# Performance work log

Hardware: AMD Instinct MI355X
Metric: run time of the kernel (lower is better)

Reference implementation:

```python
import jax, jax.numpy as jnp
import numpy as np

HEADS = 4


def setup_inputs() -> dict:
    key = jax.random.key(0)
    kx, kqkv, kbq, ko, kbo = jax.random.split(key, 5)
    B, C, H, W = 4, 256, 64, 64
    x = jax.random.normal(kx, (B, C, H, W), dtype=jnp.float32)
    # torch nn.Linear stores weight as [out_features, in_features]
    w_qkv = jax.random.normal(kqkv, (3 * C, C), dtype=jnp.float32) * (1.0 / np.sqrt(C))
    b_qkv = jax.random.normal(kbq, (3 * C,), dtype=jnp.float32) * 0.02
    w_o = jax.random.normal(ko, (C, C), dtype=jnp.float32) * (1.0 / np.sqrt(C))
    b_o = jax.random.normal(kbo, (C,), dtype=jnp.float32) * 0.02
    return {"x": x, "w_qkv": w_qkv, "b_qkv": b_qkv, "w_o": w_o, "b_o": b_o}


def reference(x, w_qkv, b_qkv, w_o, b_o):
    B, C, H, W = x.shape
    S = H * W
    hd = C // HEADS
    # (B, C, H, W) -> (B, S, C)
    xt = x.reshape(B, C, S).transpose(0, 2, 1)
    qkv = xt @ w_qkv.T + b_qkv                      # (B, S, 3C)
    q, k, v = jnp.split(qkv, 3, axis=-1)
    def to_heads(t):
        return t.reshape(B, S, HEADS, hd).transpose(0, 2, 1, 3)  # (B, h, S, hd)
    q, k, v = to_heads(q), to_heads(k), to_heads(v)
    scores = jnp.einsum('bhqd,bhkd->bhqk', q, k) / jnp.sqrt(jnp.float32(hd))
    attn = jax.nn.softmax(scores, axis=-1)          # dropout inactive (eval)
    out = jnp.einsum('bhqk,bhkd->bhqd', attn, v)    # (B, h, S, hd)
    out = out.transpose(0, 2, 1, 3).reshape(B, S, C)
    y = out @ w_o.T + b_o                            # (B, S, C)
    y = y.reshape(B, H, W, C).transpose(0, 3, 1, 2)  # (B, C, H, W)
    return y
```

## Files before the change

### kernel.cpp

```cpp
#include <hip/hip_runtime.h>
#include <stdint.h>

#define DI __device__ __forceinline__

typedef __attribute__((ext_vector_type(8))) __bf16 bf16x8;
typedef __attribute__((ext_vector_type(8))) unsigned short u16x8;
typedef __attribute__((ext_vector_type(4))) float f32x4;
typedef __attribute__((ext_vector_type(4))) uint32_t u32x4;
typedef unsigned short u16;

constexpr int Bb = 4, Cc = 256, Ss = 4096, HD = 64;
constexpr int ELEMS = Bb * Cc * Ss;

DI float bf2f(u16 h) { union { unsigned u; float f; } x; x.u = ((unsigned)h) << 16; return x.f; }
DI u16 f2bf(float f) {
  union { float f; unsigned u; } x; x.f = f;
  return (u16)((x.u + 0x7FFFu + ((x.u >> 16) & 1u)) >> 16);
}
DI uint32_t pack2bf_trunc(float a, float b) {
  union { float f; uint32_t u; } xa, xb;
  xa.f = a; xb.f = b;
  return __builtin_amdgcn_perm(xb.u, xa.u, 0x07060302u);
}
DI bf16x8 ldfrag(const u16* p) { return __builtin_bit_cast(bf16x8, *(const u16x8*)p); }

__global__ __launch_bounds__(256) void k_transpose(const float* __restrict__ x, u16* __restrict__ xt,
                                                   const float* __restrict__ wq, const float* __restrict__ wo,
                                                   u16* __restrict__ wqb, u16* __restrict__ wob) {
  __shared__ u16 T[64][72];
  const int st = blockIdx.x, ct = blockIdx.y, b = blockIdx.z;
  const int tid = threadIdx.x;
  {
    int flat = blockIdx.x + 64 * blockIdx.y + 256 * blockIdx.z;
    int widx = flat * 256 + tid;
    if (widx < 196608) wqb[widx] = f2bf(wq[widx]);
    else wob[widx - 196608] = f2bf(wo[widx - 196608]);
  }
#pragma unroll
  for (int e = 0; e < 2; e++) {
    int ss = tid + e * 256;
    int r = ss >> 3, seg = ss & 7;
    size_t base = ((size_t)(b * Cc + ct * 64 + r) << 12) + st * 64 + seg * 8;
    u16x8 t;
#pragma unroll
    for (int j = 0; j < 8; j++) t[j] = f2bf(x[base + j]);
    *(u16x8*)&T[r][(seg ^ ((r >> 3) & 7)) * 8] = t;
  }
  __syncthreads();
#pragma unroll
  for (int e = 0; e < 2; e++) {
    int ss = tid + e * 256;
    int sr = ss >> 3, cseg = ss & 7;
    u16x8 o;
#pragma unroll
    for (int j = 0; j < 8; j++) {
      int row = cseg * 8 + j;
      o[j] = T[row][(((sr >> 3) ^ cseg) * 8) + (sr & 7)];
    }
    *(u16x8*)(xt + ((size_t)(b * Ss + st * 64 + sr) << 8) + ct * 64 + cseg * 8) = o;
  }
}

DI void stage_tile(const u16* __restrict__ src, int pitch, int r0, int k0, u16 (*dst)[40], int tid) {
#pragma unroll
  for (int e = 0; e < 2; e++) {
    int c = tid + e * 256;
    int row = c >> 2, seg = c & 3;
    u16x8 t = *(const u16x8*)(src + (size_t)(r0 + row) * pitch + k0 + seg * 8);
    *(u16x8*)&dst[row][seg * 8] = t;
  }
}

__global__ __launch_bounds__(256) void k_qkv(const u16* __restrict__ xt, const u16* __restrict__ w,
                                             const float* __restrict__ bias,
                                             u16* __restrict__ q, u16* __restrict__ kk_, u16* __restrict__ vv_) {
  __shared__ u16 As[128][40], Bs[128][40];
  const int tid = threadIdx.x;
  const int wv = tid >> 6, lane = tid & 63;
  const int wm = wv >> 1, wn = wv & 1;
  const int lr = lane & 15, quad = lane >> 4;
  const int r0 = blockIdx.x * 128;
  const int j0 = blockIdx.y * 128;
  f32x4 acc[4][4] = {};
  for (int k0 = 0; k0 < 256; k0 += 32) {
    __syncthreads();
    stage_tile(xt, 256, r0, k0, As, tid);
    stage_tile(w, 256, j0, k0, Bs, tid);
    __syncthreads();
    bf16x8 a[4], b[4];
#pragma unroll
    for (int mt = 0; mt < 4; mt++) a[mt] = ldfrag(&As[wm * 64 + mt * 16 + lr][quad * 8]);
#pragma unroll
    for (int nt = 0; nt < 4; nt++) b[nt] = ldfrag(&Bs[wn * 64 + nt * 16 + lr][quad * 8]);
#pragma unroll
    for (int mt = 0; mt < 4; mt++)
#pragma unroll
      for (int nt = 0; nt < 4; nt++)
        acc[mt][nt] = __builtin_amdgcn_mfma_f32_16x16x32_bf16(a[mt], b[nt], acc[mt][nt], 0, 0, 0);
  }
#pragma unroll
  for (int nt = 0; nt < 4; nt++) {
    int j = j0 + wn * 64 + nt * 16 + lr;
    float bj = bias[j];
    int part = j >> 8, cc = j & 255, head = cc >> 6, d = cc & 63;
    u16* outp = (part == 0) ? q : (part == 1) ? kk_ : vv_;
    float sc = (part == 0) ? 0.18033688f : 1.0f;
#pragma unroll
    for (int mt = 0; mt < 4; mt++)
#pragma unroll
      for (int rg = 0; rg < 4; rg++) {
        int row = r0 + wm * 64 + mt * 16 + quad * 4 + rg;
        int b_ = row >> 12, s = row & 4095;
        outp[((size_t)((b_ * 4 + head) * Ss + s) << 6) + d] = f2bf((acc[mt][nt][rg] + bj) * sc);
      }
  }
}

__global__ __launch_bounds__(256) void k_vt(const u16* __restrict__ v, u16* __restrict__ vt) {
  __shared__ u16 T[64][72];
  const int chunk = blockIdx.x, bh = blockIdx.y;
  const int tid = threadIdx.x;
#pragma unroll
  for (int e = 0; e < 2; e++) {
    int row = (tid >> 3) + e * 32, seg = tid & 7;
    *(u16x8*)&T[row][(seg ^ ((row >> 3) & 7)) * 8] =
        *(const u16x8*)(v + ((size_t)(bh * Ss + chunk * 64 + row) << 6) + seg * 8);
  }
  __syncthreads();
#pragma unroll
  for (int e = 0; e < 2; e++) {
    int d = (tid >> 3) + e * 32, seg = tid & 7;
    u16x8 o;
#pragma unroll
    for (int j = 0; j < 8; j++) {
      int slot = seg * 8 + j;
      int t = (((slot >> 5) & 1) << 1) | ((slot >> 2) & 1);
      int w6 = t * 16 + (((slot >> 3) & 3) << 2) + (slot & 3);
      o[j] = T[w6][(((d >> 3) ^ ((w6 >> 3) & 7)) * 8) + (d & 7)];
    }
    *(u16x8*)(vt + ((size_t)(bh * 64 + d) << 12) + chunk * 64 + seg * 8) = o;
  }
}

__global__ __launch_bounds__(256, 2) void k_attn(const u16* __restrict__ Q, const u16* __restrict__ K,
                                                 const u16* __restrict__ VT, u16* __restrict__ AO,
                                                 u16* __restrict__ AOP, float* __restrict__ lpart,
                                                 int nsplit) {
  __shared__ u16 Kl[2][64][64];
  __shared__ u16 Vl[2][64][64];
  const int tid = threadIdx.x;
  const int wv = tid >> 6, lane = tid & 63;
  const int lr = lane & 15, quad = lane >> 4;
  const int bh = blockIdx.y;
  const int b_ = bh >> 2, head = bh & 3;
  const int qbase = blockIdx.x * 256 + wv * 64;
  const int sp = blockIdx.z;
  const int nchunk = 64 / nsplit, kcg0 = sp * nchunk;
  const u16* Qh = Q + (size_t)bh * Ss * HD;
  const u16* Kh = K + (size_t)bh * Ss * HD;
  const u16* Vh = VT + (size_t)bh * HD * Ss;

  bf16x8 qb[4][2];
#pragma unroll
  for (int nt = 0; nt < 4; nt++)
#pragma unroll
    for (int ks = 0; ks < 2; ks++)
      qb[nt][ks] = ldfrag(Qh + (size_t)(qbase + nt * 16 + lr) * HD + ks * 32 + quad * 8);

  u16x8 ov;
#pragma unroll
  for (int j = 0; j < 8; j++) ov[j] = 0x3F80;
  const bf16x8 ones = __builtin_bit_cast(bf16x8, ov);

  f32x4 O[4][4] = {};
  f32x4 lacc[4] = {};

  u16x8 pf[4];
  const int srow = tid >> 3, sseg = tid & 7;
  const int sg = (sseg ^ (srow & 7)) * 8;
  auto load_chunk = [&](int kc) {
#pragma unroll
    for (int e = 0; e < 2; e++) {
      pf[e] = *(const u16x8*)(Kh + ((size_t)((kcg0 + kc) * 64 + srow + e * 32) << 6) + sseg * 8);
      pf[2 + e] = *(const u16x8*)(Vh + ((size_t)(srow + e * 32) << 12) + (kcg0 + kc) * 64 + sseg * 8);
    }
  };
  auto store_chunk = [&](int buf) {
#pragma unroll
    for (int e = 0; e < 2; e++) {
      *(u16x8*)&Kl[buf][srow + e * 32][sg] = pf[e];
      *(u16x8*)&Vl[buf][srow + e * 32][sg] = pf[2 + e];
    }
  };

  load_chunk(0);
  store_chunk(0);
  if (nchunk > 1) load_chunk(1);
  __syncthreads();

  for (int kc = 0; kc < nchunk; kc++) {
    const int cur = kc & 1;
    if (kc + 1 < nchunk) {
      store_chunk(cur ^ 1);
      if (kc + 2 < nchunk) load_chunk(kc + 2);
    }

    f32x4 St[4][4] = {};
#pragma unroll
    for (int ks = 0; ks < 2; ks++) {
      bf16x8 ka[4];
#pragma unroll
      for (int kt = 0; kt < 4; kt++) {
        int g = ((ks * 4 + quad) ^ (lr & 7)) * 8;
        ka[kt] = ldfrag(&Kl[cur][kt * 16 + lr][g]);
      }
      __builtin_amdgcn_s_setprio(1);
#pragma unroll
      for (int kt = 0; kt < 4; kt++)
#pragma unroll
        for (int nt = 0; nt < 4; nt++)
          St[kt][nt] = __builtin_amdgcn_mfma_f32_16x16x32_bf16(ka[kt], qb[nt][ks], St[kt][nt], 0, 0, 0);
      __builtin_amdgcn_s_setprio(0);
    }

    uint32_t pk[4][4][2];
#pragma unroll
    for (int kt = 0; kt < 4; kt++)
#pragma unroll
      for (int nt = 0; nt < 4; nt++) {
        float p0 = __builtin_amdgcn_exp2f(St[kt][nt][0]);
        float p1 = __builtin_amdgcn_exp2f(St[kt][nt][1]);
        float p2 = __builtin_amdgcn_exp2f(St[kt][nt][2]);
        float p3 = __builtin_amdgcn_exp2f(St[kt][nt][3]);
        pk[kt][nt][0] = pack2bf_trunc(p0, p1);
        pk[kt][nt][1] = pack2bf_trunc(p2, p3);
      }

#pragma unroll
    for (int ks = 0; ks < 2; ks++) {
      bf16x8 pa[4];
#pragma unroll
      for (int mt = 0; mt < 4; mt++) {
        u32x4 t = {pk[2 * ks][mt][0], pk[2 * ks][mt][1], pk[2 * ks + 1][mt][0], pk[2 * ks + 1][mt][1]};
        pa[mt] = __builtin_bit_cast(bf16x8, t);
      }
#pragma unroll
      for (int dt = 0; dt < 4; dt++) {
        int g = ((ks * 4 + quad) ^ (lr & 7)) * 8;
        bf16x8 vb = ldfrag(&Vl[cur][dt * 16 + lr][g]);
        __builtin_amdgcn_s_setprio(1);
#pragma unroll
        for (int mt = 0; mt < 4; mt++)
          O[mt][dt] = __builtin_amdgcn_mfma_f32_16x16x32_bf16(pa[mt], vb, O[mt][dt], 0, 0, 0);
        __builtin_amdgcn_s_setprio(0);
      }
#pragma unroll
      for (int mt = 0; mt < 4; mt++)
        lacc[mt] = __builtin_amdgcn_mfma_f32_16x16x32_bf16(pa[mt], ones, lacc[mt], 0, 0, 0);
    }

    __syncthreads();
  }

  u16* dst = (nsplit == 1) ? AO : (AOP + (size_t)sp * ELEMS);
  if (nsplit > 1 && lr == 0) {
    float* lp = lpart + (size_t)sp * (16 * Ss) + bh * Ss;
#pragma unroll
    for (int mt = 0; mt < 4; mt++)
#pragma unroll
      for (int rg = 0; rg < 4; rg++) lp[qbase + mt * 16 + quad * 4 + rg] = lacc[mt][rg];
  }
#pragma unroll
  for (int mt = 0; mt < 4; mt++)
#pragma unroll
    for (int rg = 0; rg < 4; rg++) {
      float inv = 1.0f / lacc[mt][rg];
      int s = qbase + mt * 16 + quad * 4 + rg;
#pragma unroll
      for (int dt = 0; dt < 4; dt++)
        dst[((size_t)(b_ * Ss + s) << 8) + head * 64 + dt * 16 + lr] = f2bf(O[mt][dt][rg] * inv);
    }
}

__global__ __launch_bounds__(256) void k_oproj(const u16* __restrict__ wo, const u16* __restrict__ ao,
                                               const u16* __restrict__ AOP, const float* __restrict__ lpart,
                                               const float* __restrict__ bo, float* __restrict__ y, int nsplit) {
  __shared__ u16 As[128][40], Bs[128][40];
  const int tid = threadIdx.x;
  const int wv = tid >> 6, lane = tid & 63;
  const int wm = wv >> 1, wn = wv & 1;
  const int lr = lane & 15, quad = lane >> 4;
  const int n0 = blockIdx.x * 128;
  const int m0 = blockIdx.y * 128;
  f32x4 acc[4][4] = {};
  for (int k0 = 0; k0 < 256; k0 += 32) {
    __syncthreads();
    stage_tile(wo, 256, m0, k0, As, tid);
#pragma unroll
    for (int e = 0; e < 2; e++) {
      int c = tid + e * 256;
      int row = c >> 2, seg = c & 3;
      int bs = n0 + row, cc = k0 + seg * 8;
      u16x8 t;
      if (nsplit == 1) {
        t = *(const u16x8*)(ao + ((size_t)bs << 8) + cc);
      } else {
        int b = bs >> 12, s = bs & 4095, head = cc >> 6;
        int li = (b * 4 + head) * Ss + s;
        float accv[8] = {0.f, 0.f, 0.f, 0.f, 0.f, 0.f, 0.f, 0.f};
        float lsum = 0.f;
        for (int spl = 0; spl < nsplit; spl++) {
          float l = lpart[(size_t)spl * (16 * Ss) + li];
          u16x8 a = *(const u16x8*)(AOP + (size_t)spl * ELEMS + ((size_t)bs << 8) + cc);
          lsum += l;
#pragma unroll
          for (int i = 0; i < 8; i++) accv[i] += l * bf2f(a[i]);
        }
        float inv = 1.0f / lsum;
#pragma unroll
        for (int i = 0; i < 8; i++) t[i] = f2bf(accv[i] * inv);
      }
      *(u16x8*)&Bs[row][seg * 8] = t;
    }
    __syncthreads();
    bf16x8 a[4], b[4];
#pragma unroll
    for (int mt = 0; mt < 4; mt++) a[mt] = ldfrag(&As[wm * 64 + mt * 16 + lr][quad * 8]);
#pragma unroll
    for (int nt = 0; nt < 4; nt++) b[nt] = ldfrag(&Bs[wn * 64 + nt * 16 + lr][quad * 8]);
#pragma unroll
    for (int mt = 0; mt < 4; mt++)
#pragma unroll
      for (int nt = 0; nt < 4; nt++)
        acc[mt][nt] = __builtin_amdgcn_mfma_f32_16x16x32_bf16(a[mt], b[nt], acc[mt][nt], 0, 0, 0);
  }
#pragma unroll
  for (int mt = 0; mt < 4; mt++)
#pragma unroll
    for (int rg = 0; rg < 4; rg++) {
      int c = m0 + wm * 64 + mt * 16 + quad * 4 + rg;
      float bc = bo[c];
#pragma unroll
      for (int nt = 0; nt < 4; nt++) {
        int col = n0 + wn * 64 + nt * 16 + lr;
        int b_ = col >> 12, s = col & 4095;
        y[((size_t)(b_ * Cc + c) << 12) + s] = acc[mt][nt][rg] + bc;
      }
    }
}

extern "C" void kernel_launch(void* const* d_in, const int* in_sizes, int n_in,
                              void* d_out, int out_size, void* d_ws, size_t ws_size,
                              hipStream_t stream) {
  const float* x = (const float*)d_in[0];
  const float* w_qkv = (const float*)d_in[1];
  const float* b_qkv = (const float*)d_in[2];
  const float* w_o = (const float*)d_in[3];
  const float* b_o = (const float*)d_in[4];
  float* y = (float*)d_out;
  u16* ws = (u16*)d_ws;
  u16* xt = ws;
  u16* q = ws + (size_t)ELEMS;
  u16* k = ws + (size_t)2 * ELEMS;
  u16* vt = ws + (size_t)3 * ELEMS;
  u16* ao = xt;
  u16* wqb = ws + (size_t)4 * ELEMS;
  u16* wob = wqb + 196608;
  const size_t Wu16 = (size_t)4 * ELEMS + 262144;
  auto need = [&](int n) { return (Wu16 + (size_t)n * ELEMS) * 2 + (size_t)n * 16 * Ss * 4; };
  const int nsplit = (ws_size >= need(4)) ? 4 : (ws_size >= need(2)) ? 2 : 1;
  u16* aop = ws + Wu16;
  u16* v = aop;
  float* lpart = (float*)(aop + (size_t)nsplit * ELEMS);

  k_transpose<<<dim3(64, 4, 4), 256, 0, stream>>>(x, xt, w_qkv, w_o, wqb, wob);
  k_qkv<<<dim3(128, 6), 256, 0, stream>>>(xt, wqb, b_qkv, q, k, v);
  k_vt<<<dim3(64, 16), 256, 0, stream>>>(v, vt);
  k_attn<<<dim3(16, 16, nsplit), 256, 0, stream>>>(q, k, vt, ao, aop, lpart, nsplit);
  k_oproj<<<dim3(128, 2), 256, 0, stream>>>(wob, ao, aop, lpart, b_o, y, nsplit);
}
```

Baseline: 189.0 us.

## Stage K/V tiles with direct global-to-LDS loads and interleave QK/softmax/PV per half

Replaces the register-staged K/V prefetch (global load into registers, then LDS store) with global_load_lds direct copies into the double-buffered LDS tiles. The per-chunk compute is restructured to process the 64 keys in two halves: QK^T, exp2 and pack for 32 keys, then the PV MFMAs, instead of materializing all 16 score tiles at once. This cuts register pressure, and launch bounds are raised to 3 waves per SIMD to allow higher occupancy. The risk is that direct-to-LDS loads need proper waitcnt handling before the barrier, and that the finer interleaving may reduce MFMA issue density.

```diff
diff --git a/kernel.cpp b/kernel.cpp
--- a/kernel.cpp
+++ b/kernel.cpp
@@ -23,6 +23,11 @@
   return __builtin_amdgcn_perm(xb.u, xa.u, 0x07060302u);
 }
 DI bf16x8 ldfrag(const u16* p) { return __builtin_bit_cast(bf16x8, *(const u16x8*)p); }
+
+DI void g2l16(const u16* g, u16* l) {
+  __builtin_amdgcn_global_load_lds((const __attribute__((address_space(1))) uint32_t*)(const void*)g,
+                                   (__attribute__((address_space(3))) uint32_t*)(void*)l, 16, 0, 0);
+}
 
 __global__ __launch_bounds__(256) void k_transpose(const float* __restrict__ x, u16* __restrict__ xt,
                                                    const float* __restrict__ wq, const float* __restrict__ wo,
@@ -142,7 +147,7 @@
   }
 }
 
-__global__ __launch_bounds__(256, 2) void k_attn(const u16* __restrict__ Q, const u16* __restrict__ K,
+__global__ __launch_bounds__(256, 3) void k_attn(const u16* __restrict__ Q, const u16* __restrict__ K,
                                                  const u16* __restrict__ VT, u16* __restrict__ AO,
                                                  u16* __restrict__ AOP, float* __restrict__ lpart,
                                                  int nsplit) {
@@ -175,79 +180,64 @@
   f32x4 O[4][4] = {};
   f32x4 lacc[4] = {};
 
-  u16x8 pf[4];
-  const int srow = tid >> 3, sseg = tid & 7;
-  const int sg = (sseg ^ (srow & 7)) * 8;
-  auto load_chunk = [&](int kc) {
-#pragma unroll
-    for (int e = 0; e < 2; e++) {
-      pf[e] = *(const u16x8*)(Kh + ((size_t)((kcg0 + kc) * 64 + srow + e * 32) << 6) + sseg * 8);
-      pf[2 + e] = *(const u16x8*)(Vh + ((size_t)(srow + e * 32) << 12) + (kcg0 + kc) * 64 + sseg * 8);
-    }
+  const int lrow = lane >> 3;
+  const int lseg = ((lane & 7) ^ lrow) * 8;
+  const int kd0 = wv * 16 + lrow;
+  const u16* pK0 = Kh + ((size_t)(kcg0 * 64 + kd0) << 6) + lseg;
+  const u16* pK1 = pK0 + (8 << 6);
+  const u16* pV0 = Vh + ((size_t)kd0 << 12) + kcg0 * 64 + lseg;
+  const u16* pV1 = pV0 + ((size_t)8 << 12);
+  auto stage = [&](int buf) {
+    g2l16(pK0, &Kl[buf][wv * 16][0]);
+    g2l16(pK1, &Kl[buf][wv * 16 + 8][0]);
+    g2l16(pV0, &Vl[buf][wv * 16][0]);
+    g2l16(pV1, &Vl[buf][wv * 16 + 8][0]);
+    pK0 += 4096; pK1 += 4096; pV0 += 64; pV1 += 64;
   };
-  auto store_chunk = [&](int buf) {
-#pragma unroll
-    for (int e = 0; e < 2; e++) {
-      *(u16x8*)&Kl[buf][srow + e * 32][sg] = pf[e];
-      *(u16x8*)&Vl[buf][srow + e * 32][sg] = pf[2 + e];
-    }
-  };
-
-  load_chunk(0);
-  store_chunk(0);
-  if (nchunk > 1) load_chunk(1);
+
+  stage(0);
   __syncthreads();
 
   for (int kc = 0; kc < nchunk; kc++) {
     const int cur = kc & 1;
-    if (kc + 1 < nchunk) {
-      store_chunk(cur ^ 1);
-      if (kc + 2 < nchunk) load_chunk(kc + 2);
-    }
-
-    f32x4 St[4][4] = {};
-#pragma unroll
-    for (int ks = 0; ks < 2; ks++) {
-      bf16x8 ka[4];
-#pragma unroll
-      for (int kt = 0; kt < 4; kt++) {
-        int g = ((ks * 4 + quad) ^ (lr & 7)) * 8;
-        ka[kt] = ldfrag(&Kl[cur][kt * 16 + lr][g]);
-      }
-      __builtin_amdgcn_s_setprio(1);
-#pragma unroll
-      for (int kt = 0; kt < 4; kt++)
+    if (kc + 1 < nchunk) stage(cur ^ 1);
+
+#pragma unroll
+    for (int h = 0; h < 2; h++) {
+      uint32_t pk[2][4][2];
+#pragma unroll
+      for (int kt2 = 0; kt2 < 2; kt2++) {
+        const int krow = (h * 2 + kt2) * 16 + lr;
+        bf16x8 ka0 = ldfrag(&Kl[cur][krow][(quad ^ (lr & 7)) * 8]);
+        bf16x8 ka1 = ldfrag(&Kl[cur][krow][((4 + quad) ^ (lr & 7)) * 8]);
+        f32x4 St[4] = {};
+        __builtin_amdgcn_s_setprio(1);
 #pragma unroll
         for (int nt = 0; nt < 4; nt++)
-          St[kt][nt] = __builtin_amdgcn_mfma_f32_16x16x32_bf16(ka[kt], qb[nt][ks], St[kt][nt], 0, 0, 0);
-      __builtin_amdgcn_s_setprio(0);
-    }
-
-    uint32_t pk[4][4][2];
-#pragma unroll
-    for (int kt = 0; kt < 4; kt++)
-#pragma unroll
-      for (int nt = 0; nt < 4; nt++) {
-        float p0 = __builtin_amdgcn_exp2f(St[kt][nt][0]);
-        float p1 = __builtin_amdgcn_exp2f(St[kt][nt][1]);
-        float p2 = __builtin_amdgcn_exp2f(St[kt][nt][2]);
-        float p3 = __builtin_amdgcn_exp2f(St[kt][nt][3]);
-        pk[kt][nt][0] = pack2bf_trunc(p0, p1);
-        pk[kt][nt][1] = pack2bf_trunc(p2, p3);
-      }
-
-#pragma unroll
-    for (int ks = 0; ks < 2; ks++) {
+          St[nt] = __builtin_amdgcn_mfma_f32_16x16x32_bf16(ka0, qb[nt][0], St[nt], 0, 0, 0);
+#pragma unroll
+        for (int nt = 0; nt < 4; nt++)
+          St[nt] = __builtin_amdgcn_mfma_f32_16x16x32_bf16(ka1, qb[nt][1], St[nt], 0, 0, 0);
+        __builtin_amdgcn_s_setprio(0);
+#pragma unroll
+        for (int nt = 0; nt < 4; nt++) {
+          float p0 = __builtin_amdgcn_exp2f(St[nt][0]);
+          float p1 = __builtin_amdgcn_exp2f(St[nt][1]);
+          float p2 = __builtin_amdgcn_exp2f(St[nt][2]);
+          float p3 = __builtin_amdgcn_exp2f(St[nt][3]);
+          pk[kt2][nt][0] = pack2bf_trunc(p0, p1);
+          pk[kt2][nt][1] = pack2bf_trunc(p2, p3);
+        }
+      }
       bf16x8 pa[4];
 #pragma unroll
       for (int mt = 0; mt < 4; mt++) {
-        u32x4 t = {pk[2 * ks][mt][0], pk[2 * ks][mt][1], pk[2 * ks + 1][mt][0], pk[2 * ks + 1][mt][1]};
+        u32x4 t = {pk[0][mt][0], pk[0][mt][1], pk[1][mt][0], pk[1][mt][1]};
         pa[mt] = __builtin_bit_cast(bf16x8, t);
       }
 #pragma unroll
       for (int dt = 0; dt < 4; dt++) {
-        int g = ((ks * 4 + quad) ^ (lr & 7)) * 8;
-        bf16x8 vb = ldfrag(&Vl[cur][dt * 16 + lr][g]);
+        bf16x8 vb = ldfrag(&Vl[cur][dt * 16 + lr][((h * 4 + quad) ^ (lr & 7)) * 8]);
         __builtin_amdgcn_s_setprio(1);
 #pragma unroll
         for (int mt = 0; mt < 4; mt++)
```

Measured after the change: 188.8 us. About the same (-0.1%).
